# Kernel tuning notes

Measured on AMD Instinct MI355X. Metric: run time of the kernel, lower is better.

Reference implementation:

```python
import jax, jax.numpy as jnp
import numpy as np

N = 262144
IN_DIM = 256
HIDDEN = 256
NUM_SEG = 1024


def setup_inputs() -> dict:
    key = jax.random.key(0)
    k1, k2, k3, k4, k5, k6 = jax.random.split(key, 6)
    x = jax.random.normal(k1, (N, IN_DIM), dtype=jnp.float32)
    batch = jnp.sort(jax.random.randint(k2, (N,), 0, NUM_SEG)).astype(jnp.int64)
    s1 = 1.0 / np.sqrt(IN_DIM)
    s2 = 1.0 / np.sqrt(HIDDEN)
    W1 = jax.random.uniform(k3, (IN_DIM, HIDDEN), jnp.float32, -s1, s1)
    b1 = jax.random.uniform(k4, (HIDDEN,), jnp.float32, -s1, s1)
    W2 = jax.random.uniform(k5, (HIDDEN, 1), jnp.float32, -s2, s2)
    b2 = jax.random.uniform(k6, (1,), jnp.float32, -s2, s2)
    return {"x": x, "W1": W1, "b1": b1, "W2": W2, "b2": b2, "batch": batch}


def reference(x, W1, b1, W2, b2, batch):
    # gate MLP: Linear -> ReLU -> Linear(->1), squeeze
    h = jnp.maximum(x @ W1 + b1, 0.0)            # [N, H]
    scores = (h @ W2 + b2)[:, 0]                  # [N]
    # segment max; torch scatter_reduce 'amax' into zeros includes the
    # initial 0, so the effective max is clamped at >= 0
    seg_max = jax.ops.segment_max(scores, batch, num_segments=NUM_SEG)
    seg_max = jnp.maximum(seg_max, 0.0)           # [G]
    w = jnp.exp(scores - seg_max[batch])          # [N]
    seg_sum = jax.ops.segment_sum(w, batch, num_segments=NUM_SEG)  # [G]
    w = w / (seg_sum[batch] + 1e-9)               # [N]
    out = jax.ops.segment_sum(x * w[:, None], batch, num_segments=NUM_SEG)  # [G, D]
    return out
```

## Files before the change

kernel.cpp:

```cpp
#include <hip/hip_runtime.h>
#include <stdint.h>

typedef __attribute__((ext_vector_type(8))) short short8;
typedef __attribute__((ext_vector_type(4))) float f32x4;

static constexpr int kN   = 262144;
static constexpr int kD   = 256;
static constexpr int kSeg = 1024;
static constexpr int kRS  = 260;
static constexpr int kNB  = kN / 32;

__device__ __forceinline__ unsigned short f2bf(float f) {
    union { float f; unsigned int u; } v; v.f = f;
    unsigned int u = v.u;
    return (unsigned short)((u + 0x7FFFu + ((u >> 16) & 1u)) >> 16);
}

__device__ __forceinline__ void gload_lds16(const float* gsrc, float* lds_dst) {
    __builtin_amdgcn_global_load_lds(
        (const __attribute__((address_space(1))) void*)gsrc,
        (__attribute__((address_space(3))) void*)lds_dst,
        16, 0, 0);
}

__global__ void pack_w1_kernel(const float* __restrict__ W1, unsigned short* __restrict__ packed) {
    int t = blockIdx.x * blockDim.x + threadIdx.x;
    int l = t & 63, kk = (t >> 6) & 7, j = t >> 9;
    int col = j * 16 + (l & 15);
    int kb  = kk * 32 + ((l >> 4) & 3) * 8;
    short8 s;
#pragma unroll
    for (int i = 0; i < 8; ++i) s[i] = (short)f2bf(W1[(size_t)(kb + i) * kD + col]);
    *reinterpret_cast<short8*>(packed + (size_t)t * 8) = s;
}

__global__ __launch_bounds__(256, 4) void score_accum_kernel(
    const float* __restrict__ x, const unsigned short* __restrict__ packedW1,
    const float* __restrict__ b1, const float* __restrict__ W2,
    const float* __restrict__ b2, const int* __restrict__ batch,
    float* __restrict__ partial_x, float* __restrict__ partial_w,
    int* __restrict__ slot_seg)
{
    __shared__ float sx[32 * kRS];
    __shared__ float sred[4][32];
    __shared__ float sw[32];
    __shared__ int   sseg[32];

    const int tid  = threadIdx.x;
    const int lane = tid & 63;
    const int wave = tid >> 6;
    const int r0   = lane & 15;
    const int q    = lane >> 4;
    const int block_row = blockIdx.x * 32;

    if (tid < 32) sseg[tid] = batch[block_row + tid];

    {
        const float* src = x + (size_t)(block_row + wave * 8) * kD + lane * 4;
#pragma unroll
        for (int r = 0; r < 8; ++r)
            gload_lds16(src + (size_t)r * kD, &sx[(wave * 8 + r) * kRS]);
    }
    asm volatile("s_waitcnt vmcnt(0)" ::: "memory");
    __syncthreads();

    short8 afrag[2][8];
#pragma unroll
    for (int rt = 0; rt < 2; ++rt) {
        const float* rp = &sx[(rt * 16 + r0) * kRS + q * 8];
#pragma unroll
        for (int kk = 0; kk < 8; ++kk) {
            f32x4 v0 = *reinterpret_cast<const f32x4*>(rp + kk * 32);
            f32x4 v1 = *reinterpret_cast<const f32x4*>(rp + kk * 32 + 4);
            short8 a;
            a[0] = (short)f2bf(v0[0]); a[1] = (short)f2bf(v0[1]);
            a[2] = (short)f2bf(v0[2]); a[3] = (short)f2bf(v0[3]);
            a[4] = (short)f2bf(v1[0]); a[5] = (short)f2bf(v1[1]);
            a[6] = (short)f2bf(v1[2]); a[7] = (short)f2bf(v1[3]);
            afrag[rt][kk] = a;
        }
    }

    float spart[2][4] = {{0.f,0.f,0.f,0.f},{0.f,0.f,0.f,0.f}};
    const short8* bbase = reinterpret_cast<const short8*>(packedW1);
#pragma unroll
    for (int jj = 0; jj < 4; ++jj) {
        const int j = wave * 4 + jj;
        short8 bfrag[8];
        const short8* bp = bbase + (size_t)(j * 8) * 64 + lane;
#pragma unroll
        for (int kk = 0; kk < 8; ++kk) bfrag[kk] = bp[(size_t)kk * 64];
        const int col16 = j * 16 + r0;
        const float b1c = b1[col16];
        const float w2c = W2[col16];
#pragma unroll
        for (int rt = 0; rt < 2; ++rt) {
            f32x4 acc = {0.f, 0.f, 0.f, 0.f};
#pragma unroll
            for (int kk = 0; kk < 8; ++kk)
                acc = __builtin_amdgcn_mfma_f32_16x16x32_bf16(afrag[rt][kk], bfrag[kk], acc, 0, 0, 0);
#pragma unroll
            for (int r = 0; r < 4; ++r) {
                float h = fmaxf(acc[r] + b1c, 0.f);
                spart[rt][r] = fmaf(h, w2c, spart[rt][r]);
            }
        }
    }

#pragma unroll
    for (int rt = 0; rt < 2; ++rt)
#pragma unroll
        for (int r = 0; r < 4; ++r) {
            float vv = spart[rt][r];
            vv += __shfl_xor(vv, 1);
            vv += __shfl_xor(vv, 2);
            vv += __shfl_xor(vv, 4);
            vv += __shfl_xor(vv, 8);
            if (r0 == 0) sred[wave][rt * 16 + q * 4 + r] = vv;
        }
    __syncthreads();
    if (tid < 32) {
        float s = sred[0][tid] + sred[1][tid] + sred[2][tid] + sred[3][tid] + b2[0];
        sw[tid] = __expf(s);
    }
    __syncthreads();

    const int base = blockIdx.x * 2;
    int   cur = sseg[0], slot = 0;
    float acc = 0.f, wsum = 0.f;
    for (int i = 0; i < 32; ++i) {
        const float wv = sw[i];
        const int   sg = sseg[i];
        if (sg != cur) {
            partial_x[(size_t)(base + slot) * kD + tid] = acc;
            if (tid == 0) { partial_w[base + slot] = wsum; slot_seg[base + slot] = cur; }
            slot = (slot < 1) ? slot + 1 : 1;
            acc = 0.f; wsum = 0.f; cur = sg;
        }
        acc  = fmaf(sx[i * kRS + tid], wv, acc);
        wsum += wv;
    }
    partial_x[(size_t)(base + slot) * kD + tid] = acc;
    if (tid == 0) {
        partial_w[base + slot] = wsum;
        slot_seg[base + slot]  = cur;
        if (slot == 0) slot_seg[base + 1] = -1;
    }
}

__global__ __launch_bounds__(256) void reduce_kernel(
    const int* __restrict__ batch, const float* __restrict__ partial_x,
    const float* __restrict__ partial_w, const int* __restrict__ slot_seg,
    float* __restrict__ out)
{
    const int g   = blockIdx.x;
    const int tid = threadIdx.x;
    __shared__ int sb[2];
    if (tid < 2) {
        int target = g + tid;
        int lo = 0, hi = kN;
        while (lo < hi) {
            int mid = (lo + hi) >> 1;
            if (batch[mid] < target) lo = mid + 1; else hi = mid;
        }
        sb[tid] = lo;
    }
    __syncthreads();
    const int lo = sb[0], hi = sb[1];

    float acc = 0.f, wsum = 0.f;
    if (hi > lo) {
        const int b0 = lo >> 5, b1 = (hi - 1) >> 5;
        for (int b = b0; b <= b1; ++b) {
#pragma unroll
            for (int s = 0; s < 2; ++s) {
                const int idx = b * 2 + s;
                if (slot_seg[idx] == g) {
                    acc  += partial_x[(size_t)idx * kD + tid];
                    wsum += partial_w[idx];
                }
            }
        }
    }
    out[(size_t)g * kD + tid] = acc / (wsum + 1e-9f);
}

extern "C" void kernel_launch(void* const* d_in, const int* in_sizes, int n_in,
                              void* d_out, int out_size, void* d_ws, size_t ws_size,
                              hipStream_t stream) {
    const float* x     = (const float*)d_in[0];
    const float* W1    = (const float*)d_in[1];
    const float* b1    = (const float*)d_in[2];
    const float* W2    = (const float*)d_in[3];
    const float* b2    = (const float*)d_in[4];
    const int*   batch = (const int*)d_in[5];
    float* out = (float*)d_out;

    char* ws = (char*)d_ws;
    unsigned short* packed  = (unsigned short*)ws;
    float* partial_x = (float*)(ws + (1u << 17));
    float* partial_w = (float*)(ws + (1u << 17) + (1u << 24));
    int*   slot_seg  = (int*)  (ws + (1u << 17) + (1u << 24) + (1u << 16));

    pack_w1_kernel<<<32, 256, 0, stream>>>(W1, packed);
    score_accum_kernel<<<kNB, 256, 0, stream>>>(x, packed, b1, W2, b2, batch,
                                                partial_x, partial_w, slot_seg);
    reduce_kernel<<<kSeg, 256, 0, stream>>>(batch, partial_x, partial_w, slot_seg, out);
}
```

Baseline: 427.6 us.

## Stage x tile in LDS as bf16 via register loads to raise occupancy

The x tile is now loaded from global memory into registers, converted to bf16, and stored to LDS at half the footprint, replacing the direct global-to-LDS fp32 copy. MFMA A fragments are read straight from the bf16 LDS tile instead of being preconverted into registers, and launch bounds request 8 blocks per CU. The intent is to cut LDS use and registers so more blocks fit per CU and latency is better hidden. The trade-off is that the weighted segment accumulation now uses bf16-rounded x instead of fp32 x, which lowers output precision.

```diff
diff --git a/kernel.cpp b/kernel.cpp
--- a/kernel.cpp
+++ b/kernel.cpp
@@ -3,24 +3,18 @@
 
 typedef __attribute__((ext_vector_type(8))) short short8;
 typedef __attribute__((ext_vector_type(4))) float f32x4;
+typedef __attribute__((ext_vector_type(4))) unsigned short u16x4;
 
 static constexpr int kN   = 262144;
 static constexpr int kD   = 256;
 static constexpr int kSeg = 1024;
-static constexpr int kRS  = 260;
+static constexpr int kCS  = 264;
 static constexpr int kNB  = kN / 32;
 
 __device__ __forceinline__ unsigned short f2bf(float f) {
     union { float f; unsigned int u; } v; v.f = f;
     unsigned int u = v.u;
     return (unsigned short)((u + 0x7FFFu + ((u >> 16) & 1u)) >> 16);
-}
-
-__device__ __forceinline__ void gload_lds16(const float* gsrc, float* lds_dst) {
-    __builtin_amdgcn_global_load_lds(
-        (const __attribute__((address_space(1))) void*)gsrc,
-        (__attribute__((address_space(3))) void*)lds_dst,
-        16, 0, 0);
 }
 
 __global__ void pack_w1_kernel(const float* __restrict__ W1, unsigned short* __restrict__ packed) {
@@ -34,14 +28,14 @@
     *reinterpret_cast<short8*>(packed + (size_t)t * 8) = s;
 }
 
-__global__ __launch_bounds__(256, 4) void score_accum_kernel(
+__global__ __launch_bounds__(256, 8) void score_accum_kernel(
     const float* __restrict__ x, const unsigned short* __restrict__ packedW1,
     const float* __restrict__ b1, const float* __restrict__ W2,
     const float* __restrict__ b2, const int* __restrict__ batch,
     float* __restrict__ partial_x, float* __restrict__ partial_w,
     int* __restrict__ slot_seg)
 {
-    __shared__ float sx[32 * kRS];
+    __shared__ unsigned short xb[32 * kCS];
     __shared__ float sred[4][32];
     __shared__ float sw[32];
     __shared__ int   sseg[32];
@@ -55,31 +49,20 @@
 
     if (tid < 32) sseg[tid] = batch[block_row + tid];
 
-    {
-        const float* src = x + (size_t)(block_row + wave * 8) * kD + lane * 4;
+    const float* xt = x + (size_t)block_row * kD;
+    f32x4 v[8];
 #pragma unroll
-        for (int r = 0; r < 8; ++r)
-            gload_lds16(src + (size_t)r * kD, &sx[(wave * 8 + r) * kRS]);
+    for (int k = 0; k < 8; ++k)
+        v[k] = *reinterpret_cast<const f32x4*>(xt + k * 1024 + tid * 4);
+#pragma unroll
+    for (int k = 0; k < 8; ++k) {
+        const int row = 4 * k + wave;
+        u16x4 h;
+        h[0] = f2bf(v[k][0]); h[1] = f2bf(v[k][1]);
+        h[2] = f2bf(v[k][2]); h[3] = f2bf(v[k][3]);
+        *reinterpret_cast<u16x4*>(&xb[row * kCS + lane * 4]) = h;
     }
-    asm volatile("s_waitcnt vmcnt(0)" ::: "memory");
     __syncthreads();
-
-    short8 afrag[2][8];
-#pragma unroll
-    for (int rt = 0; rt < 2; ++rt) {
-        const float* rp = &sx[(rt * 16 + r0) * kRS + q * 8];
-#pragma unroll
-        for (int kk = 0; kk < 8; ++kk) {
-            f32x4 v0 = *reinterpret_cast<const f32x4*>(rp + kk * 32);
-            f32x4 v1 = *reinterpret_cast<const f32x4*>(rp + kk * 32 + 4);
-            short8 a;
-            a[0] = (short)f2bf(v0[0]); a[1] = (short)f2bf(v0[1]);
-            a[2] = (short)f2bf(v0[2]); a[3] = (short)f2bf(v0[3]);
-            a[4] = (short)f2bf(v1[0]); a[5] = (short)f2bf(v1[1]);
-            a[6] = (short)f2bf(v1[2]); a[7] = (short)f2bf(v1[3]);
-            afrag[rt][kk] = a;
-        }
-    }
 
     float spart[2][4] = {{0.f,0.f,0.f,0.f},{0.f,0.f,0.f,0.f}};
     const short8* bbase = reinterpret_cast<const short8*>(packedW1);
@@ -95,10 +78,13 @@
         const float w2c = W2[col16];
 #pragma unroll
         for (int rt = 0; rt < 2; ++rt) {
+            const unsigned short* ap = &xb[(rt * 16 + r0) * kCS + q * 8];
             f32x4 acc = {0.f, 0.f, 0.f, 0.f};
 #pragma unroll
-            for (int kk = 0; kk < 8; ++kk)
-                acc = __builtin_amdgcn_mfma_f32_16x16x32_bf16(afrag[rt][kk], bfrag[kk], acc, 0, 0, 0);
+            for (int kk = 0; kk < 8; ++kk) {
+                short8 a = *reinterpret_cast<const short8*>(ap + kk * 32);
+                acc = __builtin_amdgcn_mfma_f32_16x16x32_bf16(a, bfrag[kk], acc, 0, 0, 0);
+            }
 #pragma unroll
             for (int r = 0; r < 4; ++r) {
                 float h = fmaxf(acc[r] + b1c, 0.f);
@@ -134,10 +120,11 @@
         if (sg != cur) {
             partial_x[(size_t)(base + slot) * kD + tid] = acc;
             if (tid == 0) { partial_w[base + slot] = wsum; slot_seg[base + slot] = cur; }
-            slot = (slot < 1) ? slot + 1 : 1;
+            slot = 1;
             acc = 0.f; wsum = 0.f; cur = sg;
         }
-        acc  = fmaf(sx[i * kRS + tid], wv, acc);
+        unsigned int u = xb[i * kCS + tid];
+        acc  = fmaf(__uint_as_float(u << 16), wv, acc);
         wsum += wv;
     }
     partial_x[(size_t)(base + slot) * kD + tid] = acc;
```

New measurement: 434.2 us. No clear change (+1.5%).
